# Performance work log

Hardware: AMD Instinct MI355X
Metric: run time of the kernel (lower is better)

Reference implementation:

```python
import jax, jax.numpy as jnp
import numpy as np

T, B, V, E, H = 256, 64, 10000, 400, 1152


def _n(k, shape, scale=0.05):
    return jax.random.normal(k, shape, jnp.float32) * scale


def setup_inputs() -> dict:
    key = jax.random.key(0)
    ks = jax.random.split(key, 32)
    inp = {}
    inp["x"] = jax.random.randint(ks[0], (T, B), 0, V)
    inp["h0"] = _n(ks[1], (B, H)); inp["h1"] = _n(ks[2], (B, H)); inp["h2"] = _n(ks[3], (B, E))
    inp["c0"] = _n(ks[4], (B, H)); inp["c1"] = _n(ks[5], (B, H)); inp["c2"] = _n(ks[6], (B, E))
    inp["emb"] = _n(ks[7], (V, E), 0.1)
    # layer i: (input_dim, output_dim): (E,H), (H,H), (H,E)
    sizes = [(E, H), (H, H), (H, E)]
    j = 8
    for i, (din, dout) in enumerate(sizes):
        inp[f"W_ih{i}"] = _n(ks[j], (4 * dout, din)); j += 1
        inp[f"W_hh{i}"] = _n(ks[j], (4 * dout, dout)); j += 1
        inp[f"b_ih{i}"] = _n(ks[j], (4 * dout,)); j += 1
        inp[f"b_hh{i}"] = _n(ks[j], (4 * dout,)); j += 1
    inp["dec_W"] = _n(ks[j], (V, E)); j += 1
    inp["dec_b"] = jnp.zeros((V,), jnp.float32)
    return inp


def lstm_cell(x, h, c, Wih, Whh, bih, bhh):
    # PyTorch LSTMCell: gates = x@Wih^T + bih + h@Whh^T + bhh, order i,f,g,o
    g = x @ Wih.T + h @ Whh.T + bih + bhh
    i, f, gg, o = jnp.split(g, 4, axis=-1)
    c2 = jax.nn.sigmoid(f) * c + jax.nn.sigmoid(i) * jnp.tanh(gg)
    h2 = jax.nn.sigmoid(o) * jnp.tanh(c2)
    return h2, c2


def reference(x, h0, h1, h2, c0, c1, c2, emb,
              W_ih0, W_hh0, b_ih0, b_hh0,
              W_ih1, W_hh1, b_ih1, b_hh1,
              W_ih2, W_hh2, b_ih2, b_hh2,
              dec_W, dec_b):
    xe = emb[x]  # [T, B, E]

    def step(carry, xt):
        a0, a1, a2, s0, s1, s2 = carry
        a0, s0 = lstm_cell(xt, a0, s0, W_ih0, W_hh0, b_ih0, b_hh0)
        a1, s1 = lstm_cell(a0, a1, s1, W_ih1, W_hh1, b_ih1, b_hh1)
        a2, s2 = lstm_cell(a1, a2, s2, W_ih2, W_hh2, b_ih2, b_hh2)
        return (a0, a1, a2, s0, s1, s2), a2

    _, out = jax.lax.scan(step, (h0, h1, h2, c0, c1, c2), xe)  # out: [T, B, E]
    decoded = out @ dec_W.T + dec_b  # [T, B, V]
    return decoded
```

## Files before the change

kernel.cpp:

```cpp
#include <hip/hip_runtime.h>
#include <hip/hip_bf16.h>

typedef __hip_bfloat16 bf16;
typedef __attribute__((ext_vector_type(8))) short short8;
typedef __attribute__((ext_vector_type(4))) float f32x4;

#define T_ 256
#define B_ 64
#define V_ 10000
#define E_ 400
#define H_ 1152
#define KU 2304
#define XW 416
#define KD 416
#define XET (XW*B_)
#define NBLK 169

#define MFMA16 __builtin_amdgcn_mfma_f32_16x16x32_bf16
#define ATL(p) __hip_atomic_load((p), __ATOMIC_RELAXED, __HIP_MEMORY_SCOPE_AGENT)
#define ATS(p, v) __hip_atomic_store((p), (v), __ATOMIC_RELAXED, __HIP_MEMORY_SCOPE_AGENT)
#define PIN(x) asm volatile("" : "+v"(x))


__global__ __launch_bounds__(256) void prep_wint8(
    const float* __restrict__ s1, int w1,
    const float* __restrict__ s2, int off2, int w2, int Hl,
    bf16* __restrict__ dst, long total8)
{
    long i = (long)blockIdx.x * 256 + threadIdx.x;
    if (i >= total8) return;
    const int KB = KU / 8;
    int kb = (int)(i % KB) * 8;
    long r = i / KB;
    int hcol = (int)(r >> 2), gate = (int)(r & 3);
    long srow = (long)gate * Hl + hcol;
    const float* src = nullptr;
    if (kb < w1) src = s1 + srow * w1 + kb;
    else if (kb >= off2 && kb < off2 + w2) src = s2 + srow * w2 + (kb - off2);
    short8 v;
    #pragma unroll
    for (int j = 0; j < 8; ++j) {
        bf16 b = __float2bfloat16(src ? src[j] : 0.f);
        unsigned short us; __builtin_memcpy(&us, &b, 2);
        v[j] = (short)us;
    }
    *(short8*)(dst + r * KU + kb) = v;
}

__global__ __launch_bounds__(256) void prep_wcat8(
    const float* __restrict__ s1, int w1,
    bf16* __restrict__ dst, int Ktot, long total8)
{
    long i = (long)blockIdx.x * 256 + threadIdx.x;
    if (i >= total8) return;
    int KB = Ktot / 8;
    int kb = (int)(i % KB) * 8;
    long n = i / KB;
    const float* src = (kb < w1) ? s1 + n * w1 + kb : nullptr;
    short8 v;
    #pragma unroll
    for (int j = 0; j < 8; ++j) {
        bf16 b = __float2bfloat16(src ? src[j] : 0.f);
        unsigned short us; __builtin_memcpy(&us, &b, 2);
        v[j] = (short)us;
    }
    *(short8*)(dst + n * Ktot + kb) = v;
}

__global__ __launch_bounds__(256) void bias_int(
    const float* __restrict__ a, const float* __restrict__ b,
    int Hl, float* __restrict__ d, int n)
{
    int r = blockIdx.x * 256 + threadIdx.x;
    if (r >= n) return;
    int hcol = r >> 2, gate = r & 3;
    d[r] = a[gate * Hl + hcol] + b[gate * Hl + hcol];
}

__global__ __launch_bounds__(256) void gather_xef8(
    const int* __restrict__ x, const float* __restrict__ emb,
    bf16* __restrict__ XEf)
{
    long i = (long)blockIdx.x * 256 + threadIdx.x;
    const long total8 = (long)T_ * B_ * (XW / 8);
    if (i >= total8) return;
    const int KB = XW / 8;
    int kb = (int)(i % KB) * 8;
    int b = (int)((i / KB) % B_);
    int t = (int)(i / ((long)KB * B_));
    const float* src = (kb < E_) ? emb + (long)x[t * B_ + b] * E_ + kb : nullptr;
    short8 v;
    #pragma unroll
    for (int j = 0; j < 8; ++j) {
        bf16 bb = __float2bfloat16(src ? src[j] : 0.f);
        unsigned short us; __builtin_memcpy(&us, &bb, 2);
        v[j] = (short)us;
    }
    *(short8*)(XEf + (long)t * XET + (((kb >> 3) * 64 + b) << 3)) = v;
}

__global__ __launch_bounds__(256) void copy_hf(
    const float* __restrict__ src, bf16* __restrict__ dst, int cols, int total)
{
    int i = blockIdx.x * 256 + threadIdx.x;
    if (i >= total) return;
    int k = i % cols, b = i / cols;
    dst[(((k >> 3) * 64 + b) << 3) + (k & 7)] = __float2bfloat16(src[(long)b * cols + k]);
}

__global__ __launch_bounds__(256) void copy_f32(
    const float* __restrict__ src, float* __restrict__ dst, int n)
{
    int i = blockIdx.x * 256 + threadIdx.x;
    if (i < n) dst[i] = src[i];
}

__device__ __forceinline__ void grid_bar(int* flags, int* gen, int phase) {
    asm volatile("s_waitcnt vmcnt(0)" ::: "memory");
    __syncthreads();
    if (blockIdx.x == 0) {
        if (threadIdx.x < 64) {
            const int ln = threadIdx.x;
            if (ln == 0) ATS(&flags[0], phase);
            for (;;) {
                int f0 = (ln       < NBLK) ? ATL(&flags[ln])       : phase;
                int f1 = (ln + 64  < NBLK) ? ATL(&flags[ln + 64])  : phase;
                int f2 = (ln + 128 < NBLK) ? ATL(&flags[ln + 128]) : phase;
                if (__all(f0 >= phase && f1 >= phase && f2 >= phase)) break;
                __builtin_amdgcn_s_sleep(1);
            }
            if (ln == 0) {
                ATS(gen, phase);
                __builtin_amdgcn_fence(__ATOMIC_ACQUIRE, "agent");
            }
        }
    } else {
        if (threadIdx.x == 0) {
            ATS(&flags[blockIdx.x], phase);
            while (ATL(gen) < phase)
                __builtin_amdgcn_s_sleep(1);
            __builtin_amdgcn_fence(__ATOMIC_ACQUIRE, "agent");
        }
    }
    __syncthreads();
    asm volatile("" ::: "memory");
}

struct Frag4 { short8 f0, f1, f2, f3; };

__global__ __launch_bounds__(512, 2) void awd_persistent(
    const bf16* __restrict__ XEf,
    const bf16* __restrict__ W0, const bf16* __restrict__ W1, const bf16* __restrict__ W2,
    const float* __restrict__ b0, const float* __restrict__ b1, const float* __restrict__ b2,
    bf16* H0f0, bf16* H0f1, bf16* H1f0, bf16* H1f1, bf16* H2f0, bf16* H2f1,
    float* c0, float* c1, float* c2, bf16* OUTB,
    int* flags, int* gen)
{
    __shared__ float gsm[2][4][64][65];
    __shared__ unsigned short hsm[64][24];
    const int bid = blockIdx.x;
    const int tid = threadIdx.x;
    const int lane = tid & 63;
    const int w8 = tid >> 6;
    const int lh = lane >> 4, l15 = lane & 15;
    const int boff8 = (lh * 64 + l15) * 8;

    int layer, grp;
    if (bid < 72)       { layer = 1; grp = bid; }
    else if (bid < 144) { layer = 0; grp = bid - 72; }
    else                { layer = 2; grp = bid - 144; }

    const bf16* Wp  = (layer == 0) ? W0 : (layer == 1) ? W1 : W2;
    const float* bias = (layer == 0) ? b0 : (layer == 1) ? b1 : b2;
    const float* cbuf = (layer == 0) ? c0 : (layer == 1) ? c1 : c2;
    const int Hl  = (layer == 2) ? 400 : 1152;
    const int bkt = (layer == 0) ? 13 : 36;
    const int nkt = (layer == 1) ? 72 : 49;
    const int KT  = (layer == 1) ? 9  : 7;
    const int kbase = w8 * KT;

    short8 wreg[9][4];
    #pragma unroll
    for (int u = 0; u < 9; ++u)
        if (u < KT) {
            #pragma unroll
            for (int rt = 0; rt < 4; ++rt) {
                int row = grp * 64 + rt * 16 + l15;
                int k   = (kbase + u) * 32 + lh * 8;
                wreg[u][rt] = *(const short8*)(Wp + (long)row * KU + k);
                PIN(wreg[u][rt]);
            }
        }

    float myb[2][4];
    #pragma unroll
    for (int e = 0; e < 2; ++e)
        #pragma unroll
        for (int g = 0; g < 4; ++g)
            myb[e][g] = bias[grp * 64 + (w8 + e * 8) * 4 + g];

    float creg[2];
    #pragma unroll
    for (int e = 0; e < 2; ++e)
        creg[e] = cbuf[(long)lane * Hl + grp * 16 + w8 + e * 8];

    for (int s = -1; s <= 256; ++s) {
        bool active = (layer == 0) ? (s <= 254)
                    : (layer == 1) ? (s >= 0 && s <= 255)
                                   : (s >= 1);
        if (active) {
            const int p = s & 1, q = p ^ 1;
            const bf16 *A1, *A2; bf16* hfW; bf16* ob = nullptr;
            if (layer == 0) {
                A1 = XEf + (long)(s + 1) * XET;
                A2 = p ? H0f1 : H0f0;
                hfW = q ? H0f1 : H0f0;
            } else if (layer == 1) {
                A1 = p ? H0f1 : H0f0;
                A2 = q ? H1f1 : H1f0;
                hfW = p ? H1f1 : H1f0;
            } else {
                A1 = q ? H1f1 : H1f0;
                A2 = p ? H2f1 : H2f0;
                hfW = q ? H2f1 : H2f0;
                ob = OUTB + (long)(s - 1) * B_ * XW;
            }

            auto loadf = [&](int u) -> Frag4 {
                const int ktg = kbase + u;
                const bf16* src; int ktL;
                if (ktg < bkt)      { src = A1; ktL = ktg; }
                else if (ktg < nkt) { src = A2; ktL = ktg - bkt; }
                else                { src = A1; ktL = 0; }
                const bf16* pB = src + ktL * 2048 + boff8;
                Frag4 r;
                r.f0 = *(const short8*)(pB);
                r.f1 = *(const short8*)(pB + 128);
                r.f2 = *(const short8*)(pB + 256);
                r.f3 = *(const short8*)(pB + 384);
                return r;
            };

            f32x4 acc[4][4];
            #pragma unroll
            for (int rt = 0; rt < 4; ++rt)
                #pragma unroll
                for (int m = 0; m < 4; ++m)
                    acc[rt][m] = (f32x4){0.f, 0.f, 0.f, 0.f};

            auto domfma = [&](int u, const Frag4& f) {
                #pragma unroll
                for (int rt = 0; rt < 4; ++rt) {
                    acc[rt][0] = MFMA16(wreg[u][rt], f.f0, acc[rt][0], 0, 0, 0);
                    acc[rt][1] = MFMA16(wreg[u][rt], f.f1, acc[rt][1], 0, 0, 0);
                    acc[rt][2] = MFMA16(wreg[u][rt], f.f2, acc[rt][2], 0, 0, 0);
                    acc[rt][3] = MFMA16(wreg[u][rt], f.f3, acc[rt][3], 0, 0, 0);
                }
            };

            #pragma unroll
            for (int u = 0; u < 9; ++u)
                if (u < KT) {
                    Frag4 f = loadf(u);
                    domfma(u, f);
                }

            #pragma unroll
            for (int rt = 0; rt < 4; ++rt)
                #pragma unroll
                for (int m = 0; m < 4; ++m)
                    #pragma unroll
                    for (int r = 0; r < 4; ++r)
                        gsm[w8 >> 2][w8 & 3][rt * 16 + lh * 4 + r][m * 16 + l15] = acc[rt][m][r];
            __syncthreads();

            #pragma unroll
            for (int e = 0; e < 2; ++e) {
                int b = lane;
                int cl = w8 + e * 8;
                float gv[4];
                #pragma unroll
                for (int g = 0; g < 4; ++g) {
                    float v = myb[e][g];
                    #pragma unroll
                    for (int kq = 0; kq < 4; ++kq)
                        v += gsm[0][kq][cl * 4 + g][b] + gsm[1][kq][cl * 4 + g][b];
                    gv[g] = v;
                }
                float c_old = creg[e];
                float i_s = 1.f / (1.f + expf(-gv[0]));
                float f_s = 1.f / (1.f + expf(-gv[1]));
                float o_s = 1.f / (1.f + expf(-gv[3]));
                float c_new = f_s * c_old + i_s * tanhf(gv[2]);
                float hval = o_s * tanhf(c_new);
                creg[e] = c_new;
                bf16 hb = __float2bfloat16(hval);
                unsigned short hbits;
                __builtin_memcpy(&hbits, &hb, 2);
                hsm[b][cl] = hbits;
            }
            __syncthreads();

            if (w8 < 2) {
                unsigned long long v0, v1;
                __builtin_memcpy(&v0, &hsm[lane][w8 * 8], 8);
                __builtin_memcpy(&v1, &hsm[lane][w8 * 8 + 4], 8);
                unsigned long long* qp =
                    (unsigned long long*)(hfW + (((long)grp * 2 + w8) * 64 + lane) * 8);
                ATS(qp, v0);
                ATS(qp + 1, v1);
            } else if (w8 == 2 && layer == 2) {
                short8 v0 = *(const short8*)&hsm[lane][0];
                short8 v1 = *(const short8*)&hsm[lane][8];
                *(short8*)(ob + (long)lane * XW + grp * 16) = v0;
                *(short8*)(ob + (long)lane * XW + grp * 16 + 8) = v1;
            }
        }
        grid_bar(flags, gen, s + 2);
    }
}

__global__ __launch_bounds__(256) void decoder(
    const bf16* __restrict__ A, const bf16* __restrict__ W,
    const float* __restrict__ bias, float* __restrict__ out)
{
    const int id = blockIdx.x;
    const int xcd = id & 7;
    const int local = id >> 3;
    const int n_blk = xcd * 10 + local % 10;
    const int m_blk = local / 10;
    if (n_blk >= 79) return;

    const int tid = threadIdx.x;
    const int lane = tid & 63;
    const int w = tid >> 6;
    const int mw = w >> 1, nw = w & 1;
    const int n0 = n_blk * 128 + nw * 64;
    const int m0 = m_blk * 128 + mw * 64;
    const int c16 = lane & 15;
    const int kg = lane >> 4;

    f32x4 acc[4][4];
    #pragma unroll
    for (int mi = 0; mi < 4; ++mi)
        #pragma unroll
        for (int ns = 0; ns < 4; ++ns)
            acc[mi][ns] = (f32x4){0.f, 0.f, 0.f, 0.f};

    int nrow[4];
    #pragma unroll
    for (int ns = 0; ns < 4; ++ns) {
        int n = n0 + ns * 16 + c16;
        nrow[ns] = (n < V_) ? n : (V_ - 1);
    }

    const bf16* arow = A + (long)(m0 + c16) * KD + kg * 8;
    #pragma unroll
    for (int kt = 0; kt < 13; ++kt) {
        short8 af[4], bf[4];
        #pragma unroll
        for (int mi = 0; mi < 4; ++mi)
            af[mi] = *(const short8*)(arow + (long)mi * 16 * KD + kt * 32);
        #pragma unroll
        for (int ns = 0; ns < 4; ++ns)
            bf[ns] = *(const short8*)(W + (long)nrow[ns] * KD + kt * 32 + kg * 8);
        #pragma unroll
        for (int mi = 0; mi < 4; ++mi)
            #pragma unroll
            for (int ns = 0; ns < 4; ++ns)
                acc[mi][ns] = MFMA16(af[mi], bf[ns], acc[mi][ns], 0, 0, 0);
    }

    #pragma unroll
    for (int mi = 0; mi < 4; ++mi)
        #pragma unroll
        for (int ns = 0; ns < 4; ++ns) {
            int col = n0 + ns * 16 + c16;
            if (col < V_) {
                float bv = bias[col];
                #pragma unroll
                for (int r = 0; r < 4; ++r) {
                    int row = m0 + mi * 16 + kg * 4 + r;
                    out[(size_t)row * V_ + col] = acc[mi][ns][r] + bv;
                }
            }
        }
}


extern "C" void kernel_launch(void* const* d_in, const int* in_sizes, int n_in,
                              void* d_out, int out_size, void* d_ws, size_t ws_size,
                              hipStream_t stream)
{
    const int*   x    = (const int*)d_in[0];
    const float* h0   = (const float*)d_in[1];
    const float* h1   = (const float*)d_in[2];
    const float* h2   = (const float*)d_in[3];
    const float* c0   = (const float*)d_in[4];
    const float* c1   = (const float*)d_in[5];
    const float* c2   = (const float*)d_in[6];
    const float* emb  = (const float*)d_in[7];
    const float* Wih0 = (const float*)d_in[8];
    const float* Whh0 = (const float*)d_in[9];
    const float* bih0 = (const float*)d_in[10];
    const float* bhh0 = (const float*)d_in[11];
    const float* Wih1 = (const float*)d_in[12];
    const float* Whh1 = (const float*)d_in[13];
    const float* bih1 = (const float*)d_in[14];
    const float* bhh1 = (const float*)d_in[15];
    const float* Wih2 = (const float*)d_in[16];
    const float* Whh2 = (const float*)d_in[17];
    const float* bih2 = (const float*)d_in[18];
    const float* bhh2 = (const float*)d_in[19];
    const float* decW = (const float*)d_in[20];
    const float* decb = (const float*)d_in[21];

    char* wsb = (char*)d_ws;
    size_t off = 0;
    auto alloc = [&](size_t bytes) -> void* {
        void* ptr = wsb + off;
        off = (off + bytes + 255) & ~(size_t)255;
        return ptr;
    };

    bf16* W0i = (bf16*)alloc((size_t)4608 * KU * 2);
    bf16* W1i = (bf16*)alloc((size_t)4608 * KU * 2);
    bf16* W2i = (bf16*)alloc((size_t)1600 * KU * 2);
    bf16* Wdc = (bf16*)alloc((size_t)V_ * KD * 2);
    float* b0i = (float*)alloc(4608 * 4);
    float* b1i = (float*)alloc(4608 * 4);
    float* b2i = (float*)alloc(1600 * 4);
    bf16* XEf = (bf16*)alloc((size_t)T_ * XET * 2);
    bf16* H0f0 = (bf16*)alloc((size_t)B_ * H_ * 2);
    bf16* H0f1 = (bf16*)alloc((size_t)B_ * H_ * 2);
    bf16* H1f0 = (bf16*)alloc((size_t)B_ * H_ * 2);
    bf16* H1f1 = (bf16*)alloc((size_t)B_ * H_ * 2);
    bf16* H2f0 = (bf16*)alloc((size_t)B_ * XW * 2);
    bf16* H2f1 = (bf16*)alloc((size_t)B_ * XW * 2);
    float* c0b = (float*)alloc((size_t)B_ * H_ * 4);
    float* c1b = (float*)alloc((size_t)B_ * H_ * 4);
    float* c2b = (float*)alloc((size_t)B_ * E_ * 4);
    bf16* OUTB = (bf16*)alloc((size_t)T_ * B_ * XW * 2);
    int* gbar = (int*)alloc(2048);

    auto cdiv = [](long a, long b) { return (int)((a + b - 1) / b); };

    hipMemsetAsync(gbar, 0, 2048, stream);

    prep_wint8<<<cdiv(4608L * (KU/8), 256), 256, 0, stream>>>(Wih0, 400,  Whh0, 416,  1152, 1152, W0i, 4608L * (KU/8));
    prep_wint8<<<cdiv(4608L * (KU/8), 256), 256, 0, stream>>>(Wih1, 1152, Whh1, 1152, 1152, 1152, W1i, 4608L * (KU/8));
    prep_wint8<<<cdiv(1600L * (KU/8), 256), 256, 0, stream>>>(Wih2, 1152, Whh2, 1152, 400,  400,  W2i, 1600L * (KU/8));
    prep_wcat8<<<cdiv((long)V_ * (KD/8), 256), 256, 0, stream>>>(decW, 400, Wdc, KD, (long)V_ * (KD/8));
    bias_int<<<cdiv(4608, 256), 256, 0, stream>>>(bih0, bhh0, 1152, b0i, 4608);
    bias_int<<<cdiv(4608, 256), 256, 0, stream>>>(bih1, bhh1, 1152, b1i, 4608);
    bias_int<<<cdiv(1600, 256), 256, 0, stream>>>(bih2, bhh2, 400,  b2i, 1600);
    gather_xef8<<<cdiv((long)T_ * B_ * (XW/8), 256), 256, 0, stream>>>(x, emb, XEf);

    hipMemsetAsync(H2f0, 0, (size_t)B_ * XW * 2, stream);
    hipMemsetAsync(H2f1, 0, (size_t)B_ * XW * 2, stream);
    hipMemsetAsync(OUTB, 0, (size_t)T_ * B_ * XW * 2, stream);

    copy_hf<<<cdiv(B_ * H_, 256), 256, 0, stream>>>(h0, H0f1, H_, B_ * H_);
    copy_hf<<<cdiv(B_ * H_, 256), 256, 0, stream>>>(h1, H1f1, H_, B_ * H_);
    copy_hf<<<cdiv(B_ * E_, 256), 256, 0, stream>>>(h2, H2f1, E_, B_ * E_);
    copy_f32<<<cdiv(B_ * H_, 256), 256, 0, stream>>>(c0, c0b, B_ * H_);
    copy_f32<<<cdiv(B_ * H_, 256), 256, 0, stream>>>(c1, c1b, B_ * H_);
    copy_f32<<<cdiv(B_ * E_, 256), 256, 0, stream>>>(c2, c2b, B_ * E_);

    {
        int* flags = gbar;
        int* gen   = gbar + 448;
        void* args[] = {
            (void*)&XEf, (void*)&W0i, (void*)&W1i, (void*)&W2i,
            (void*)&b0i, (void*)&b1i, (void*)&b2i,
            (void*)&H0f0, (void*)&H0f1, (void*)&H1f0, (void*)&H1f1,
            (void*)&H2f0, (void*)&H2f1,
            (void*)&c0b, (void*)&c1b, (void*)&c2b, (void*)&OUTB,
            (void*)&flags, (void*)&gen
        };
        hipLaunchCooperativeKernel((void*)awd_persistent, dim3(NBLK), dim3(512),
                                   args, 0, stream);
    }

    decoder<<<dim3(80 * 128), 256, 0, stream>>>(OUTB, Wdc, decb, (float*)d_out);
}
```

Baseline: 3.108 ms.

## Merge init kernels, spread barrier release flags, nontemporal decoder stores

Replaces three bias kernels and six state-copy kernels plus several memsets with two fused kernels, cutting launch count. The grid barrier release flag is replicated into eight cache-line-separated copies so waiting blocks poll different lines. Decoder output stores become nontemporal to avoid polluting cache with the large logits write. The changes are unrelated and mostly target launch overhead and barrier contention.

```diff
diff --git a/kernel.cpp b/kernel.cpp
--- a/kernel.cpp
+++ b/kernel.cpp
@@ -67,14 +67,23 @@
     *(short8*)(dst + n * Ktot + kb) = v;
 }
 
-__global__ __launch_bounds__(256) void bias_int(
-    const float* __restrict__ a, const float* __restrict__ b,
-    int Hl, float* __restrict__ d, int n)
-{
-    int r = blockIdx.x * 256 + threadIdx.x;
-    if (r >= n) return;
-    int hcol = r >> 2, gate = r & 3;
-    d[r] = a[gate * Hl + hcol] + b[gate * Hl + hcol];
+__global__ __launch_bounds__(256) void bias_all(
+    const float* __restrict__ bih0, const float* __restrict__ bhh0,
+    const float* __restrict__ bih1, const float* __restrict__ bhh1,
+    const float* __restrict__ bih2, const float* __restrict__ bhh2,
+    float* __restrict__ b0i, float* __restrict__ b1i, float* __restrict__ b2i)
+{
+    int i = blockIdx.x * 256 + threadIdx.x;
+    if (i < 4608) {
+        int hcol = i >> 2, g = i & 3;
+        b0i[i] = bih0[g * 1152 + hcol] + bhh0[g * 1152 + hcol];
+    } else if (i < 9216) {
+        int r = i - 4608, hcol = r >> 2, g = r & 3;
+        b1i[r] = bih1[g * 1152 + hcol] + bhh1[g * 1152 + hcol];
+    } else if (i < 10816) {
+        int r = i - 9216, hcol = r >> 2, g = r & 3;
+        b2i[r] = bih2[g * 400 + hcol] + bhh2[g * 400 + hcol];
+    }
 }
 
 __global__ __launch_bounds__(256) void gather_xef8(
@@ -99,23 +108,37 @@
     *(short8*)(XEf + (long)t * XET + (((kb >> 3) * 64 + b) << 3)) = v;
 }
 
-__global__ __launch_bounds__(256) void copy_hf(
-    const float* __restrict__ src, bf16* __restrict__ dst, int cols, int total)
+__global__ __launch_bounds__(256) void init_states(
+    const float* __restrict__ h0, const float* __restrict__ h1,
+    const float* __restrict__ h2,
+    const float* __restrict__ c0, const float* __restrict__ c1,
+    const float* __restrict__ c2,
+    bf16* __restrict__ H0f1, bf16* __restrict__ H1f1,
+    bf16* __restrict__ H2f0, bf16* __restrict__ H2f1,
+    float* __restrict__ c0b, float* __restrict__ c1b, float* __restrict__ c2b,
+    int* __restrict__ gbar)
 {
     int i = blockIdx.x * 256 + threadIdx.x;
-    if (i >= total) return;
-    int k = i % cols, b = i / cols;
-    dst[(((k >> 3) * 64 + b) << 3) + (k & 7)] = __float2bfloat16(src[(long)b * cols + k]);
-}
-
-__global__ __launch_bounds__(256) void copy_f32(
-    const float* __restrict__ src, float* __restrict__ dst, int n)
-{
-    int i = blockIdx.x * 256 + threadIdx.x;
-    if (i < n) dst[i] = src[i];
-}
-
-__device__ __forceinline__ void grid_bar(int* flags, int* gen, int phase) {
+    if (i < B_ * H_) {
+        int k = ((i >> 9) << 3) | (i & 7);
+        int b = (i >> 3) & 63;
+        H0f1[i] = __float2bfloat16(h0[(long)b * H_ + k]);
+        H1f1[i] = __float2bfloat16(h1[(long)b * H_ + k]);
+        c0b[i] = c0[i];
+        c1b[i] = c1[i];
+    }
+    if (i < B_ * XW) {
+        int k = ((i >> 9) << 3) | (i & 7);
+        int b = (i >> 3) & 63;
+        H2f1[i] = (k < E_) ? __float2bfloat16(h2[(long)b * E_ + k])
+                           : __float2bfloat16(0.f);
+        H2f0[i] = __float2bfloat16(0.f);
+    }
+    if (i < B_ * E_) c2b[i] = c2[i];
+    if (i < 512) gbar[i] = 0;
+}
+
+__device__ __forceinline__ void grid_bar(int* flags, int* gen8, int phase) {
     asm volatile("s_waitcnt vmcnt(0)" ::: "memory");
     __syncthreads();
     if (blockIdx.x == 0) {
@@ -129,15 +152,14 @@
                 if (__all(f0 >= phase && f1 >= phase && f2 >= phase)) break;
                 __builtin_amdgcn_s_sleep(1);
             }
-            if (ln == 0) {
-                ATS(gen, phase);
+            if (ln < 8) ATS(&gen8[ln * 16], phase);
+            if (ln == 0)
                 __builtin_amdgcn_fence(__ATOMIC_ACQUIRE, "agent");
-            }
         }
     } else {
         if (threadIdx.x == 0) {
             ATS(&flags[blockIdx.x], phase);
-            while (ATL(gen) < phase)
+            while (ATL(&gen8[(blockIdx.x & 7) * 16]) < phase)
                 __builtin_amdgcn_s_sleep(1);
             __builtin_amdgcn_fence(__ATOMIC_ACQUIRE, "agent");
         }
@@ -154,7 +176,7 @@
     const float* __restrict__ b0, const float* __restrict__ b1, const float* __restrict__ b2,
     bf16* H0f0, bf16* H0f1, bf16* H1f0, bf16* H1f1, bf16* H2f0, bf16* H2f1,
     float* c0, float* c1, float* c2, bf16* OUTB,
-    int* flags, int* gen)
+    int* flags, int* gen8)
 {
     __shared__ float gsm[2][4][64][65];
     __shared__ unsigned short hsm[64][24];
@@ -316,7 +338,7 @@
                 *(short8*)(ob + (long)lane * XW + grp * 16 + 8) = v1;
             }
         }
-        grid_bar(flags, gen, s + 2);
+        grid_bar(flags, gen8, s + 2);
     }
 }
 
@@ -381,7 +403,8 @@
                 #pragma unroll
                 for (int r = 0; r < 4; ++r) {
                     int row = m0 + mi * 16 + kg * 4 + r;
-                    out[(size_t)row * V_ + col] = acc[mi][ns][r] + bv;
+                    __builtin_nontemporal_store(acc[mi][ns][r] + bv,
+                                                &out[(size_t)row * V_ + col]);
                 }
             }
         }
@@ -445,38 +468,29 @@
 
     auto cdiv = [](long a, long b) { return (int)((a + b - 1) / b); };
 
-    hipMemsetAsync(gbar, 0, 2048, stream);
-
     prep_wint8<<<cdiv(4608L * (KU/8), 256), 256, 0, stream>>>(Wih0, 400,  Whh0, 416,  1152, 1152, W0i, 4608L * (KU/8));
     prep_wint8<<<cdiv(4608L * (KU/8), 256), 256, 0, stream>>>(Wih1, 1152, Whh1, 1152, 1152, 1152, W1i, 4608L * (KU/8));
     prep_wint8<<<cdiv(1600L * (KU/8), 256), 256, 0, stream>>>(Wih2, 1152, Whh2, 1152, 400,  400,  W2i, 1600L * (KU/8));
     prep_wcat8<<<cdiv((long)V_ * (KD/8), 256), 256, 0, stream>>>(decW, 400, Wdc, KD, (long)V_ * (KD/8));
-    bias_int<<<cdiv(4608, 256), 256, 0, stream>>>(bih0, bhh0, 1152, b0i, 4608);
-    bias_int<<<cdiv(4608, 256), 256, 0, stream>>>(bih1, bhh1, 1152, b1i, 4608);
-    bias_int<<<cdiv(1600, 256), 256, 0, stream>>>(bih2, bhh2, 400,  b2i, 1600);
+    bias_all<<<cdiv(10816, 256), 256, 0, stream>>>(bih0, bhh0, bih1, bhh1, bih2, bhh2, b0i, b1i, b2i);
     gather_xef8<<<cdiv((long)T_ * B_ * (XW/8), 256), 256, 0, stream>>>(x, emb, XEf);
 
-    hipMemsetAsync(H2f0, 0, (size_t)B_ * XW * 2, stream);
-    hipMemsetAsync(H2f1, 0, (size_t)B_ * XW * 2, stream);
     hipMemsetAsync(OUTB, 0, (size_t)T_ * B_ * XW * 2, stream);
 
-    copy_hf<<<cdiv(B_ * H_, 256), 256, 0, stream>>>(h0, H0f1, H_, B_ * H_);
-    copy_hf<<<cdiv(B_ * H_, 256), 256, 0, stream>>>(h1, H1f1, H_, B_ * H_);
-    copy_hf<<<cdiv(B_ * E_, 256), 256, 0, stream>>>(h2, H2f1, E_, B_ * E_);
-    copy_f32<<<cdiv(B_ * H_, 256), 256, 0, stream>>>(c0, c0b, B_ * H_);
-    copy_f32<<<cdiv(B_ * H_, 256), 256, 0, stream>>>(c1, c1b, B_ * H_);
-    copy_f32<<<cdiv(B_ * E_, 256), 256, 0, stream>>>(c2, c2b, B_ * E_);
+    init_states<<<cdiv(B_ * H_, 256), 256, 0, stream>>>(
+        h0, h1, h2, c0, c1, c2,
+        H0f1, H1f1, H2f0, H2f1, c0b, c1b, c2b, gbar);
 
     {
         int* flags = gbar;
-        int* gen   = gbar + 448;
+        int* gen8  = gbar + 256;
         void* args[] = {
             (void*)&XEf, (void*)&W0i, (void*)&W1i, (void*)&W2i,
             (void*)&b0i, (void*)&b1i, (void*)&b2i,
             (void*)&H0f0, (void*)&H0f1, (void*)&H1f0, (void*)&H1f1,
             (void*)&H2f0, (void*)&H2f1,
             (void*)&c0b, (void*)&c1b, (void*)&c2b, (void*)&OUTB,
-            (void*)&flags, (void*)&gen
+            (void*)&flags, (void*)&gen8
         };
         hipLaunchCooperativeKernel((void*)awd_persistent, dim3(NBLK), dim3(512),
                                    args, 0, stream);
```

After: 3.050 ms (median of 2 runs). Within noise of the previous version (-1.9%).
